# Optimization experiments

Hardware: AMD Instinct MI355X
Metric: run time of the kernel (lower is better)

The kernel has to match this reference:

```python
import jax, jax.numpy as jnp
import numpy as np

EMBED_DIM = 528
NUM_HEADS = 8
HEAD_DIM = EMBED_DIM // NUM_HEADS  # 66


def setup_inputs() -> dict:
    key = jax.random.key(0)
    k1, k2, k3, k4, k5 = jax.random.split(key, 5)
    B, D, H, W, C = 1, 16, 16, 16, EMBED_DIM
    s = 1.0 / np.sqrt(C)
    return {
        "x": jax.random.normal(k1, (B, D, H, W, C), dtype=jnp.float32),
        "w_qkv": jax.random.uniform(k2, (3 * C, C), dtype=jnp.float32, minval=-s, maxval=s),
        "b_qkv": jax.random.uniform(k3, (3 * C,), dtype=jnp.float32, minval=-s, maxval=s),
        "w_proj": jax.random.uniform(k4, (C, C), dtype=jnp.float32, minval=-s, maxval=s),
        "b_proj": jax.random.uniform(k5, (C,), dtype=jnp.float32, minval=-s, maxval=s),
    }


def reference(x, w_qkv, b_qkv, w_proj, b_proj):
    B, D, H, W, C = x.shape
    N = D * H * W
    h, hd = NUM_HEADS, HEAD_DIM
    scaling = hd ** (-0.5)

    xt = x.reshape(B, N, C)
    # qkv projection: [B, N, 3C] -> [3, B, h, N, hd]
    qkv = xt @ w_qkv.T + b_qkv
    qkv = qkv.reshape(B, N, 3, h, hd).transpose(2, 0, 3, 1, 4)
    q, k, v = qkv[0], qkv[1], qkv[2]

    # full attention over all D*H*W tokens
    attn = jnp.einsum('bhqd,bhkd->bhqk', q, k) * scaling
    attn = jax.nn.softmax(attn, axis=-1)
    out = jnp.einsum('bhqk,bhkd->bhqd', attn, v)  # [B, h, N, hd]

    out = out.transpose(0, 2, 1, 3).reshape(B, N, h * hd)
    out = out @ w_proj.T + b_proj
    return out.reshape(B, D, H, W, C)
```

## Files before the change

### kernel.cpp

```cpp
#include <hip/hip_runtime.h>

typedef __attribute__((ext_vector_type(8))) short bf16x8;
typedef __attribute__((ext_vector_type(4))) float f32x4;
typedef __attribute__((ext_vector_type(16))) float f32x16;

#define DEV __device__ __forceinline__

static constexpr int N_TOK = 4096;
static constexpr int C     = 528;
static constexpr int NH    = 8;
static constexpr int HD    = 66;
static constexpr int HDP   = 96;
static constexpr int VD96  = 96;
static constexpr int KP    = 544;
static constexpr int NQKV  = 1584;
static constexpr int NQKVP = 1632;

DEV unsigned short f2bf(float f) {
    unsigned int u = __float_as_uint(f);
    u = (u + 0x7fffu + ((u >> 16) & 1u)) >> 16;
    return (unsigned short)u;
}
DEV float bf2f(unsigned short h) { return __uint_as_float(((unsigned int)h) << 16); }
DEV unsigned cvtpk2(float a, float b) {
    unsigned r;
    asm("v_cvt_pk_bf16_f32 %0, %1, %2" : "=v"(r) : "v"(a), "v"(b));
    return r;
}
DEV void plswap(unsigned &a, unsigned &b) {
    asm volatile("v_permlane32_swap_b32 %0, %1" : "+v"(a), "+v"(b));
}

__global__ void k_prep_all(const float* __restrict__ x, const float* __restrict__ w_qkv,
                           const float* __restrict__ w_proj,
                           unsigned short* __restrict__ xb, unsigned short* __restrict__ wqkvb,
                           unsigned short* __restrict__ whi, unsigned short* __restrict__ wlo) {
    const int T0 = N_TOK * KP;
    const int T1 = T0 + NQKVP * KP;
    const int T2 = T1 + KP * KP;
    for (int idx = blockIdx.x * 256 + threadIdx.x; idx < T2; idx += gridDim.x * 256) {
        if (idx < T0) {
            int n = idx / KP, k = idx - n * KP;
            xb[idx] = (k < C) ? f2bf(x[n * C + k]) : (unsigned short)0;
        } else if (idx < T1) {
            int j = idx - T0;
            int n = j / KP, k = j - n * KP;
            wqkvb[j] = (n < NQKV && k < C) ? f2bf(w_qkv[n * C + k]) : (unsigned short)0;
        } else {
            int j = idx - T1;
            int n = j / KP, k = j - n * KP;
            unsigned short hi = 0, lo = 0;
            if (n < C && k < C) {
                float v = w_proj[n * C + k];
                hi = f2bf(v);
                lo = f2bf(v - bf2f(hi));
            }
            whi[j] = hi; wlo[j] = lo;
        }
    }
}

__launch_bounds__(256)
__global__ void k_gemm_qkv(const unsigned short* __restrict__ A,
                           const unsigned short* __restrict__ B,
                           const float* __restrict__ bias,
                           unsigned short* __restrict__ Cout) {
    constexpr int LDA = 40;
    __shared__ unsigned short Al[2][128 * LDA];
    __shared__ unsigned short Bl[2][96 * LDA];
    int tid = threadIdx.x, lane = tid & 63, wid = tid >> 6;
    int m0 = blockIdx.x * 128, n0 = blockIdx.y * 96;
    int wm = (wid >> 1) * 64, wn = (wid & 1) * 48;
    int arow0 = tid >> 2, arow1 = (256 + tid) >> 2, akc = (tid & 3) * 8;
    bool bhave = tid < 128;
    int brow1 = (256 + tid) >> 2;
    f32x4 acc[4][3] = {};
    bf16x8 ra0, ra1, rb0, rb1;

    ra0 = *(const bf16x8*)&A[(size_t)(m0 + arow0) * KP + akc];
    ra1 = *(const bf16x8*)&A[(size_t)(m0 + arow1) * KP + akc];
    rb0 = *(const bf16x8*)&B[(size_t)(n0 + arow0) * KP + akc];
    if (bhave) rb1 = *(const bf16x8*)&B[(size_t)(n0 + brow1) * KP + akc];
    *(bf16x8*)&Al[0][arow0 * LDA + akc] = ra0;
    *(bf16x8*)&Al[0][arow1 * LDA + akc] = ra1;
    *(bf16x8*)&Bl[0][arow0 * LDA + akc] = rb0;
    if (bhave) *(bf16x8*)&Bl[0][brow1 * LDA + akc] = rb1;
    __syncthreads();

    int kk = (lane >> 4) * 8, cc = lane & 15;
    for (int kt = 0; kt < 17; kt++) {
        int cur = kt & 1;
        if (kt < 16) {
            int k0 = (kt + 1) * 32;
            ra0 = *(const bf16x8*)&A[(size_t)(m0 + arow0) * KP + k0 + akc];
            ra1 = *(const bf16x8*)&A[(size_t)(m0 + arow1) * KP + k0 + akc];
            rb0 = *(const bf16x8*)&B[(size_t)(n0 + arow0) * KP + k0 + akc];
            if (bhave) rb1 = *(const bf16x8*)&B[(size_t)(n0 + brow1) * KP + k0 + akc];
        }
        bf16x8 af[4], bfr[3];
#pragma unroll
        for (int mi = 0; mi < 4; mi++) af[mi] = *(const bf16x8*)&Al[cur][(wm + mi * 16 + cc) * LDA + kk];
#pragma unroll
        for (int ni = 0; ni < 3; ni++) bfr[ni] = *(const bf16x8*)&Bl[cur][(wn + ni * 16 + cc) * LDA + kk];
#pragma unroll
        for (int mi = 0; mi < 4; mi++)
#pragma unroll
            for (int ni = 0; ni < 3; ni++)
                acc[mi][ni] = __builtin_amdgcn_mfma_f32_16x16x32_bf16(af[mi], bfr[ni], acc[mi][ni], 0, 0, 0);
        if (kt < 16) {
            int nxt = cur ^ 1;
            *(bf16x8*)&Al[nxt][arow0 * LDA + akc] = ra0;
            *(bf16x8*)&Al[nxt][arow1 * LDA + akc] = ra1;
            *(bf16x8*)&Bl[nxt][arow0 * LDA + akc] = rb0;
            if (bhave) *(bf16x8*)&Bl[nxt][brow1 * LDA + akc] = rb1;
        }
        __syncthreads();
    }
#pragma unroll
    for (int mi = 0; mi < 4; mi++)
#pragma unroll
        for (int ni = 0; ni < 3; ni++)
#pragma unroll
            for (int r = 0; r < 4; r++) {
                int row = m0 + wm + mi * 16 + (lane >> 4) * 4 + r;
                int col = n0 + wn + ni * 16 + cc;
                float v = acc[mi][ni][r] + (col < NQKV ? bias[col] : 0.f);
                Cout[(size_t)row * NQKVP + col] = f2bf(v);
            }
}

__global__ void k_reshape(const unsigned short* __restrict__ T,
                          unsigned short* __restrict__ qb, unsigned short* __restrict__ kbuf,
                          unsigned short* __restrict__ vt) {
    int h = blockIdx.y, n0 = blockIdx.x * 64, tid = threadIdx.x;
    if (blockIdx.z == 0) {
#pragma unroll
        for (int i = 0; i < 24; i++) {
            int idx = i * 256 + tid;
            int ni = idx / 96, d = idx - ni * 96;
            unsigned short zq = 0, zk = 0;
            if (d < HD) {
                zq = T[(size_t)(n0 + ni) * NQKVP + h * HD + d];
                zk = T[(size_t)(n0 + ni) * NQKVP + C + h * HD + d];
            }
            size_t a = ((size_t)h * N_TOK + n0 + ni) * HDP + d;
            qb[a] = zq; kbuf[a] = zk;
        }
    } else {
        __shared__ unsigned short lt[64 * 104];
#pragma unroll
        for (int i = 0; i < 24; i++) {
            int idx = i * 256 + tid;
            int ni = idx / 96, d = idx - ni * 96;
            unsigned short v = 0;
            if (d < HD) v = T[(size_t)(n0 + ni) * NQKVP + 2 * C + h * HD + d];
            lt[ni * 104 + d] = v;
        }
        __syncthreads();
#pragma unroll
        for (int i = 0; i < 24; i++) {
            int idx = i * 256 + tid;
            int d = idx >> 6, ni = idx & 63;
            vt[((size_t)h * VD96 + d) * N_TOK + n0 + ni] = lt[ni * 104 + d];
        }
    }
}

__launch_bounds__(512, 2)
__global__ void k_attn(const unsigned short* __restrict__ qb,
                       const unsigned short* __restrict__ kb,
                       const unsigned short* __restrict__ vt,
                       unsigned short* __restrict__ ahi,
                       unsigned short* __restrict__ alo) {
    __shared__ __align__(16) unsigned short Kl[2][128 * 128];
    __shared__ __align__(16) unsigned short Vl[2][96 * 128];
    int tid = threadIdx.x, lane = tid & 63, wid = tid >> 6;
    int wq = wid & 3, kh = wid >> 2;
    int hi = lane >> 5, lq = lane & 31;
    int bid = blockIdx.x;
    int head = bid & 7;
    int q0 = (bid >> 3) * 128;
    const float SC2 = 0.12309149097933274f * 1.4426950408889634f;

    bf16x8 aq[6];
    {
        const unsigned short* qrow = qb + ((size_t)head * N_TOK + q0 + wq * 32 + lq) * HDP + hi * 8;
#pragma unroll
        for (int t = 0; t < 6; t++) aq[t] = *(const bf16x8*)&qrow[t * 16];
    }
    f32x16 o0 = {}, o1 = {}, o2 = {};
    float m_r = -3e38f, l_r = 0.f;

    const unsigned short* kg = kb + (size_t)head * N_TOK * HDP;
    const unsigned short* vg = vt + (size_t)head * VD96 * N_TOK;

#pragma unroll
    for (int i = 0; i < 3; i++) {
        int c = i * 512 + tid;
        int row = c / 12, ch = c - row * 12;
        *(bf16x8*)&Kl[0][row * 128 + ((ch ^ (row & 15)) << 3)] =
            *(const bf16x8*)&kg[(size_t)row * HDP + ch * 8];
    }
#pragma unroll
    for (int i = 0; i < 3; i++) {
        int c = i * 512 + tid;
        int row = c >> 4, ch = c & 15;
        *(bf16x8*)&Vl[0][row * 128 + ((ch ^ (row & 15)) << 3)] =
            *(const bf16x8*)&vg[(size_t)row * N_TOK + ch * 8];
    }
    __syncthreads();

    for (int kt = 0; kt < 32; kt++) {
        int cur = kt & 1;
        bf16x8 gk[3], gv[3];
        if (kt < 31) {
            int n1 = (kt + 1) * 128;
#pragma unroll
            for (int i = 0; i < 3; i++) {
                int c = i * 512 + tid;
                int row = c / 12, ch = c - row * 12;
                gk[i] = *(const bf16x8*)&kg[(size_t)(n1 + row) * HDP + ch * 8];
            }
#pragma unroll
            for (int i = 0; i < 3; i++) {
                int c = i * 512 + tid;
                int row = c >> 4, ch = c & 15;
                gv[i] = *(const bf16x8*)&vg[(size_t)row * N_TOK + n1 + ch * 8];
            }
        }

        f32x16 s0 = {}, s1 = {};
        {
            int r0 = kh * 64 + lq, r1 = r0 + 32;
#pragma unroll
            for (int t = 0; t < 6; t++) {
                bf16x8 ka0 = *(const bf16x8*)&Kl[cur][r0 * 128 + (((2 * t + hi) ^ (r0 & 15)) << 3)];
                bf16x8 ka1 = *(const bf16x8*)&Kl[cur][r1 * 128 + (((2 * t + hi) ^ (r1 & 15)) << 3)];
                s0 = __builtin_amdgcn_mfma_f32_32x32x16_bf16(ka0, aq[t], s0, 0, 0, 0);
                s1 = __builtin_amdgcn_mfma_f32_32x32x16_bf16(ka1, aq[t], s1, 0, 0, 0);
            }
        }

        float mx = s0[0];
#pragma unroll
        for (int r = 1; r < 16; r++) mx = fmaxf(mx, s0[r]);
#pragma unroll
        for (int r = 0; r < 16; r++) mx = fmaxf(mx, s1[r]);
        mx = fmaxf(mx, __shfl_xor(mx, 32, 64));
        if (!__all((mx - m_r) * SC2 <= 8.f)) {
            float mnew = fmaxf(m_r, mx);
            float fct = __builtin_amdgcn_exp2f((m_r - mnew) * SC2);
            m_r = mnew;
            l_r *= fct;
#pragma unroll
            for (int r = 0; r < 16; r++) { o0[r] *= fct; o1[r] *= fct; o2[r] *= fct; }
        }
        float nb = m_r * SC2;
        float lsum = 0.f;
#pragma unroll
        for (int r = 0; r < 16; r++) { s0[r] = __builtin_amdgcn_exp2f(__builtin_fmaf(s0[r], SC2, -nb)); lsum += s0[r]; }
#pragma unroll
        for (int r = 0; r < 16; r++) { s1[r] = __builtin_amdgcn_exp2f(__builtin_fmaf(s1[r], SC2, -nb)); lsum += s1[r]; }
        lsum += __shfl_xor(lsum, 32, 64);
        l_r += lsum;

        unsigned u0[2][4], u1[2][4];
#pragma unroll
        for (int a = 0; a < 4; a++) {
            u0[0][a] = cvtpk2(s0[4 * a + 0], s0[4 * a + 1]);
            u1[0][a] = cvtpk2(s0[4 * a + 2], s0[4 * a + 3]);
            u0[1][a] = cvtpk2(s1[4 * a + 0], s1[4 * a + 1]);
            u1[1][a] = cvtpk2(s1[4 * a + 2], s1[4 * a + 3]);
        }
#pragma unroll
        for (int kb2 = 0; kb2 < 2; kb2++)
#pragma unroll
            for (int a0 = 0; a0 < 4; a0 += 2) {
                plswap(u0[kb2][a0], u0[kb2][a0 + 1]);
                plswap(u1[kb2][a0], u1[kb2][a0 + 1]);
            }

#pragma unroll
        for (int t2 = 0; t2 < 4; t2++) {
            int kb2 = t2 >> 1, a0 = (t2 & 1) * 2;
            union { unsigned u[4]; bf16x8 v; } pf;
            pf.u[0] = u0[kb2][a0];     pf.u[1] = u1[kb2][a0];
            pf.u[2] = u0[kb2][a0 + 1]; pf.u[3] = u1[kb2][a0 + 1];
            int ch = kh * 8 + 2 * t2 + hi;
            int rv0 = lq, rv1 = 32 + lq, rv2 = 64 + lq;
            bf16x8 va0 = *(const bf16x8*)&Vl[cur][rv0 * 128 + ((ch ^ (rv0 & 15)) << 3)];
            bf16x8 va1 = *(const bf16x8*)&Vl[cur][rv1 * 128 + ((ch ^ (rv1 & 15)) << 3)];
            bf16x8 va2 = *(const bf16x8*)&Vl[cur][rv2 * 128 + ((ch ^ (rv2 & 15)) << 3)];
            o0 = __builtin_amdgcn_mfma_f32_32x32x16_bf16(va0, pf.v, o0, 0, 0, 0);
            o1 = __builtin_amdgcn_mfma_f32_32x32x16_bf16(va1, pf.v, o1, 0, 0, 0);
            o2 = __builtin_amdgcn_mfma_f32_32x32x16_bf16(va2, pf.v, o2, 0, 0, 0);
        }

        if (kt < 31) {
            int nxt = cur ^ 1;
#pragma unroll
            for (int i = 0; i < 3; i++) {
                int c = i * 512 + tid;
                int row = c / 12, ch = c - row * 12;
                *(bf16x8*)&Kl[nxt][row * 128 + ((ch ^ (row & 15)) << 3)] = gk[i];
            }
#pragma unroll
            for (int i = 0; i < 3; i++) {
                int c = i * 512 + tid;
                int row = c >> 4, ch = c & 15;
                *(bf16x8*)&Vl[nxt][row * 128 + ((ch ^ (row & 15)) << 3)] = gv[i];
            }
        }
        __syncthreads();
    }

    float* xc = (float*)&Kl[0][0];
    float* rg = xc + (size_t)(wq * 64 + lane) * 52;
    if (kh == 1) {
#pragma unroll
        for (int r = 0; r < 16; r++) rg[r] = o0[r];
#pragma unroll
        for (int r = 0; r < 16; r++) rg[16 + r] = o1[r];
#pragma unroll
        for (int r = 0; r < 16; r++) rg[32 + r] = o2[r];
        rg[48] = m_r; rg[49] = l_r;
    }
    __syncthreads();
    if (kh == 0) {
        float m1 = rg[48], l1 = rg[49];
        float m12 = fmaxf(m_r, m1);
        float f0 = __builtin_amdgcn_exp2f((m_r - m12) * SC2);
        float f1 = __builtin_amdgcn_exp2f((m1 - m12) * SC2);
        float inv = 1.f / (l_r * f0 + l1 * f1);
        int token = q0 + wq * 32 + lq;
#pragma unroll
        for (int db = 0; db < 3; db++) {
#pragma unroll
            for (int r = 0; r < 16; r++) {
                int d = db * 32 + (r & 3) + 8 * (r >> 2) + 4 * hi;
                if (d < HD) {
                    float own = (db == 0) ? o0[r] : (db == 1) ? o1[r] : o2[r];
                    float val = (own * f0 + rg[db * 16 + r] * f1) * inv;
                    unsigned short hb = f2bf(val);
                    float lo = val - bf2f(hb);
                    size_t a = (size_t)token * KP + head * HD + d;
                    ahi[a] = hb; alo[a] = f2bf(lo);
                }
            }
        }
    }
}

__launch_bounds__(256)
__global__ void k_gemm_proj(const unsigned short* __restrict__ Ahi_, const unsigned short* __restrict__ Alo_,
                            const unsigned short* __restrict__ Whi_, const unsigned short* __restrict__ Wlo_,
                            const float* __restrict__ bias, float* __restrict__ out) {
    constexpr int LDA = 40;
    __shared__ unsigned short Ah[2][128 * LDA], Aw[2][128 * LDA];
    __shared__ unsigned short Bh[2][64 * LDA],  Bw[2][64 * LDA];
    int tid = threadIdx.x, lane = tid & 63, wid = tid >> 6;
    int m0 = blockIdx.x * 128, n0 = blockIdx.y * 64;
    int wm = wid * 32;
    int arow0 = tid >> 2, arow1 = (256 + tid) >> 2, akc = (tid & 3) * 8;
    bool bok = (n0 + arow0) < KP;
    f32x4 acc[2][4] = {};
    bf16x8 rah0, rah1, ral0, ral1, rbh, rbl;
    const bf16x8 zero8 = {};

    rah0 = *(const bf16x8*)&Ahi_[(size_t)(m0 + arow0) * KP + akc];
    rah1 = *(const bf16x8*)&Ahi_[(size_t)(m0 + arow1) * KP + akc];
    ral0 = *(const bf16x8*)&Alo_[(size_t)(m0 + arow0) * KP + akc];
    ral1 = *(const bf16x8*)&Alo_[(size_t)(m0 + arow1) * KP + akc];
    rbh = bok ? *(const bf16x8*)&Whi_[(size_t)(n0 + arow0) * KP + akc] : zero8;
    rbl = bok ? *(const bf16x8*)&Wlo_[(size_t)(n0 + arow0) * KP + akc] : zero8;
    *(bf16x8*)&Ah[0][arow0 * LDA + akc] = rah0;
    *(bf16x8*)&Ah[0][arow1 * LDA + akc] = rah1;
    *(bf16x8*)&Aw[0][arow0 * LDA + akc] = ral0;
    *(bf16x8*)&Aw[0][arow1 * LDA + akc] = ral1;
    *(bf16x8*)&Bh[0][arow0 * LDA + akc] = rbh;
    *(bf16x8*)&Bw[0][arow0 * LDA + akc] = rbl;
    __syncthreads();

    int kk = (lane >> 4) * 8, cc = lane & 15;
    for (int kt = 0; kt < 17; kt++) {
        int cur = kt & 1;
        if (kt < 16) {
            int k0 = (kt + 1) * 32;
            rah0 = *(const bf16x8*)&Ahi_[(size_t)(m0 + arow0) * KP + k0 + akc];
            rah1 = *(const bf16x8*)&Ahi_[(size_t)(m0 + arow1) * KP + k0 + akc];
            ral0 = *(const bf16x8*)&Alo_[(size_t)(m0 + arow0) * KP + k0 + akc];
            ral1 = *(const bf16x8*)&Alo_[(size_t)(m0 + arow1) * KP + k0 + akc];
            rbh = bok ? *(const bf16x8*)&Whi_[(size_t)(n0 + arow0) * KP + k0 + akc] : zero8;
            rbl = bok ? *(const bf16x8*)&Wlo_[(size_t)(n0 + arow0) * KP + k0 + akc] : zero8;
        }
        bf16x8 ah[2], al[2], bh[4], bl[4];
#pragma unroll
        for (int mi = 0; mi < 2; mi++) {
            ah[mi] = *(const bf16x8*)&Ah[cur][(wm + mi * 16 + cc) * LDA + kk];
            al[mi] = *(const bf16x8*)&Aw[cur][(wm + mi * 16 + cc) * LDA + kk];
        }
#pragma unroll
        for (int ni = 0; ni < 4; ni++) {
            bh[ni] = *(const bf16x8*)&Bh[cur][(ni * 16 + cc) * LDA + kk];
            bl[ni] = *(const bf16x8*)&Bw[cur][(ni * 16 + cc) * LDA + kk];
        }
#pragma unroll
        for (int mi = 0; mi < 2; mi++)
#pragma unroll
            for (int ni = 0; ni < 4; ni++) {
                acc[mi][ni] = __builtin_amdgcn_mfma_f32_16x16x32_bf16(ah[mi], bh[ni], acc[mi][ni], 0, 0, 0);
                acc[mi][ni] = __builtin_amdgcn_mfma_f32_16x16x32_bf16(ah[mi], bl[ni], acc[mi][ni], 0, 0, 0);
                acc[mi][ni] = __builtin_amdgcn_mfma_f32_16x16x32_bf16(al[mi], bh[ni], acc[mi][ni], 0, 0, 0);
            }
        if (kt < 16) {
            int nxt = cur ^ 1;
            *(bf16x8*)&Ah[nxt][arow0 * LDA + akc] = rah0;
            *(bf16x8*)&Ah[nxt][arow1 * LDA + akc] = rah1;
            *(bf16x8*)&Aw[nxt][arow0 * LDA + akc] = ral0;
            *(bf16x8*)&Aw[nxt][arow1 * LDA + akc] = ral1;
            *(bf16x8*)&Bh[nxt][arow0 * LDA + akc] = rbh;
            *(bf16x8*)&Bw[nxt][arow0 * LDA + akc] = rbl;
        }
        __syncthreads();
    }
#pragma unroll
    for (int mi = 0; mi < 2; mi++)
#pragma unroll
        for (int ni = 0; ni < 4; ni++)
#pragma unroll
            for (int r = 0; r < 4; r++) {
                int row = m0 + wm + mi * 16 + (lane >> 4) * 4 + r;
                int col = n0 + ni * 16 + cc;
                if (col < C) out[(size_t)row * C + col] = acc[mi][ni][r] + bias[col];
            }
}

extern "C" void kernel_launch(void* const* d_in, const int* in_sizes, int n_in,
                              void* d_out, int out_size, void* d_ws, size_t ws_size,
                              hipStream_t stream) {
    const float* x      = (const float*)d_in[0];
    const float* w_qkv  = (const float*)d_in[1];
    const float* b_qkv  = (const float*)d_in[2];
    const float* w_proj = (const float*)d_in[3];
    const float* b_proj = (const float*)d_in[4];
    float* out = (float*)d_out;
    char* ws = (char*)d_ws;

    const size_t o_xb     = 0;
    const size_t o_wqkvb  = o_xb     + 4456448;
    const size_t o_whi    = o_wqkvb  + 1775616;
    const size_t o_wlo    = o_whi    + 591872;
    const size_t o_qkvtmp = o_wlo    + 591872;
    const size_t o_qbf    = o_qkvtmp + 13369344;
    const size_t o_kbf    = o_qbf    + 6291456;
    const size_t o_vt     = o_kbf    + 6291456;
    const size_t need     = o_vt + 6291456;
    if (ws_size < need) return;

    unsigned short* xb     = (unsigned short*)(ws + o_xb);
    unsigned short* wqkvb  = (unsigned short*)(ws + o_wqkvb);
    unsigned short* whi    = (unsigned short*)(ws + o_whi);
    unsigned short* wlo    = (unsigned short*)(ws + o_wlo);
    unsigned short* qkvtmp = (unsigned short*)(ws + o_qkvtmp);
    unsigned short* qbf    = (unsigned short*)(ws + o_qbf);
    unsigned short* kbf    = (unsigned short*)(ws + o_kbf);
    unsigned short* vt     = (unsigned short*)(ws + o_vt);
    unsigned short* ahi    = xb;
    unsigned short* alo    = qkvtmp;

    k_prep_all  <<<2048, 256, 0, stream>>>(x, w_qkv, w_proj, xb, wqkvb, whi, wlo);
    k_gemm_qkv  <<<dim3(N_TOK / 128, NQKVP / 96), 256, 0, stream>>>(xb, wqkvb, b_qkv, qkvtmp);
    k_reshape   <<<dim3(N_TOK / 64, NH, 2), 256, 0, stream>>>(qkvtmp, qbf, kbf, vt);
    k_attn      <<<dim3(256), 512, 0, stream>>>(qbf, kbf, vt, ahi, alo);
    k_gemm_proj <<<dim3(N_TOK / 128, 9), 256, 0, stream>>>(ahi, alo, whi, wlo, b_proj, out);
}
```

Baseline: 124.1 us.

## Scatter Q/K directly from QKV GEMM and split attention keys across 16 waves

After: 152.0 us. 22.5% more time.

```diff
diff --git a/kernel.cpp b/kernel.cpp
--- a/kernel.cpp
+++ b/kernel.cpp
@@ -34,11 +34,13 @@
 __global__ void k_prep_all(const float* __restrict__ x, const float* __restrict__ w_qkv,
                            const float* __restrict__ w_proj,
                            unsigned short* __restrict__ xb, unsigned short* __restrict__ wqkvb,
-                           unsigned short* __restrict__ whi, unsigned short* __restrict__ wlo) {
+                           unsigned short* __restrict__ whi, unsigned short* __restrict__ wlo,
+                           unsigned short* __restrict__ qb, unsigned short* __restrict__ kbuf) {
     const int T0 = N_TOK * KP;
     const int T1 = T0 + NQKVP * KP;
     const int T2 = T1 + KP * KP;
-    for (int idx = blockIdx.x * 256 + threadIdx.x; idx < T2; idx += gridDim.x * 256) {
+    const int T3 = T2 + NH * N_TOK * (HDP - HD);
+    for (int idx = blockIdx.x * 256 + threadIdx.x; idx < T3; idx += gridDim.x * 256) {
         if (idx < T0) {
             int n = idx / KP, k = idx - n * KP;
             xb[idx] = (k < C) ? f2bf(x[n * C + k]) : (unsigned short)0;
@@ -46,7 +48,7 @@
             int j = idx - T0;
             int n = j / KP, k = j - n * KP;
             wqkvb[j] = (n < NQKV && k < C) ? f2bf(w_qkv[n * C + k]) : (unsigned short)0;
-        } else {
+        } else if (idx < T2) {
             int j = idx - T1;
             int n = j / KP, k = j - n * KP;
             unsigned short hi = 0, lo = 0;
@@ -56,6 +58,11 @@
                 lo = f2bf(v - bf2f(hi));
             }
             whi[j] = hi; wlo[j] = lo;
+        } else {
+            int j = idx - T2;
+            int n = j / 30, p = j - 30 * n;
+            size_t a = (size_t)n * HDP + HD + p;
+            qb[a] = 0; kbuf[a] = 0;
         }
     }
 }
@@ -64,7 +71,8 @@
 __global__ void k_gemm_qkv(const unsigned short* __restrict__ A,
                            const unsigned short* __restrict__ B,
                            const float* __restrict__ bias,
-                           unsigned short* __restrict__ Cout) {
+                           unsigned short* __restrict__ qb, unsigned short* __restrict__ kbuf,
+                           unsigned short* __restrict__ vtmp) {
     constexpr int LDA = 40;
     __shared__ unsigned short Al[2][128 * LDA];
     __shared__ unsigned short Bl[2][96 * LDA];
@@ -125,55 +133,46 @@
                 int row = m0 + wm + mi * 16 + (lane >> 4) * 4 + r;
                 int col = n0 + wn + ni * 16 + cc;
                 float v = acc[mi][ni][r] + (col < NQKV ? bias[col] : 0.f);
-                Cout[(size_t)row * NQKVP + col] = f2bf(v);
-            }
-}
-
-__global__ void k_reshape(const unsigned short* __restrict__ T,
-                          unsigned short* __restrict__ qb, unsigned short* __restrict__ kbuf,
-                          unsigned short* __restrict__ vt) {
+                unsigned short b = f2bf(v);
+                if (col < 2 * C) {
+                    int d5 = (col >= C) ? col - C : col;
+                    unsigned h = (unsigned)d5 / 66u;
+                    int dd = d5 - 66 * (int)h;
+                    size_t a = ((size_t)h * N_TOK + row) * HDP + dd;
+                    if (col >= C) kbuf[a] = b; else qb[a] = b;
+                } else if (col < NQKV) {
+                    vtmp[(size_t)row * C + (col - 2 * C)] = b;
+                }
+            }
+}
+
+__global__ void k_reshape_v(const unsigned short* __restrict__ vtmp, unsigned short* __restrict__ vt) {
+    __shared__ unsigned short lt[64 * 104];
     int h = blockIdx.y, n0 = blockIdx.x * 64, tid = threadIdx.x;
-    if (blockIdx.z == 0) {
-#pragma unroll
-        for (int i = 0; i < 24; i++) {
-            int idx = i * 256 + tid;
-            int ni = idx / 96, d = idx - ni * 96;
-            unsigned short zq = 0, zk = 0;
-            if (d < HD) {
-                zq = T[(size_t)(n0 + ni) * NQKVP + h * HD + d];
-                zk = T[(size_t)(n0 + ni) * NQKVP + C + h * HD + d];
-            }
-            size_t a = ((size_t)h * N_TOK + n0 + ni) * HDP + d;
-            qb[a] = zq; kbuf[a] = zk;
-        }
-    } else {
-        __shared__ unsigned short lt[64 * 104];
-#pragma unroll
-        for (int i = 0; i < 24; i++) {
-            int idx = i * 256 + tid;
-            int ni = idx / 96, d = idx - ni * 96;
-            unsigned short v = 0;
-            if (d < HD) v = T[(size_t)(n0 + ni) * NQKVP + 2 * C + h * HD + d];
-            lt[ni * 104 + d] = v;
-        }
-        __syncthreads();
-#pragma unroll
-        for (int i = 0; i < 24; i++) {
-            int idx = i * 256 + tid;
-            int d = idx >> 6, ni = idx & 63;
-            vt[((size_t)h * VD96 + d) * N_TOK + n0 + ni] = lt[ni * 104 + d];
-        }
-    }
-}
-
-__launch_bounds__(512, 2)
+#pragma unroll
+    for (int i = 0; i < 24; i++) {
+        int idx = i * 256 + tid;
+        int ni = idx / 96, d = idx - ni * 96;
+        unsigned short v = 0;
+        if (d < HD) v = vtmp[(size_t)(n0 + ni) * C + h * HD + d];
+        lt[ni * 104 + d] = v;
+    }
+    __syncthreads();
+#pragma unroll
+    for (int i = 0; i < 24; i++) {
+        int idx = i * 256 + tid;
+        int d = idx >> 6, ni = idx & 63;
+        vt[((size_t)h * VD96 + d) * N_TOK + n0 + ni] = lt[ni * 104 + d];
+    }
+}
+
+__launch_bounds__(1024, 4)
 __global__ void k_attn(const unsigned short* __restrict__ qb,
                        const unsigned short* __restrict__ kb,
                        const unsigned short* __restrict__ vt,
                        unsigned short* __restrict__ ahi,
                        unsigned short* __restrict__ alo) {
-    __shared__ __align__(16) unsigned short Kl[2][128 * 128];
-    __shared__ __align__(16) unsigned short Vl[2][96 * 128];
+    __shared__ __align__(16) unsigned short S[2][128 * 128 + 96 * 128];
     int tid = threadIdx.x, lane = tid & 63, wid = tid >> 6;
     int wq = wid & 3, kh = wid >> 2;
     int hi = lane >> 5, lq = lane & 31;
@@ -194,58 +193,53 @@
     const unsigned short* kg = kb + (size_t)head * N_TOK * HDP;
     const unsigned short* vg = vt + (size_t)head * VD96 * N_TOK;
 
-#pragma unroll
-    for (int i = 0; i < 3; i++) {
-        int c = i * 512 + tid;
-        int row = c / 12, ch = c - row * 12;
-        *(bf16x8*)&Kl[0][row * 128 + ((ch ^ (row & 15)) << 3)] =
-            *(const bf16x8*)&kg[(size_t)row * HDP + ch * 8];
-    }
-#pragma unroll
-    for (int i = 0; i < 3; i++) {
-        int c = i * 512 + tid;
-        int row = c >> 4, ch = c & 15;
-        *(bf16x8*)&Vl[0][row * 128 + ((ch ^ (row & 15)) << 3)] =
-            *(const bf16x8*)&vg[(size_t)row * N_TOK + ch * 8];
+    const unsigned short* gptr[3];
+    int gstep[3], laddr[3];
+#pragma unroll
+    for (int j = 0; j < 3; j++) {
+        int c = j * 1024 + tid;
+        if (c < 1536) {
+            int row = c / 12, ch = c - row * 12;
+            gptr[j] = kg + (size_t)row * HDP + ch * 8;
+            gstep[j] = 128 * HDP;
+            laddr[j] = row * 128 + ((ch ^ (row & 15)) << 3);
+        } else {
+            int c2 = c - 1536;
+            int row = c2 >> 4, ch = c2 & 15;
+            gptr[j] = vg + (size_t)row * N_TOK + ch * 8;
+            gstep[j] = 128;
+            laddr[j] = 128 * 128 + row * 128 + ((ch ^ (row & 15)) << 3);
+        }
+    }
+#pragma unroll
+    for (int j = 0; j < 3; j++) {
+        *(bf16x8*)&S[0][laddr[j]] = *(const bf16x8*)gptr[j];
+        gptr[j] += gstep[j];
     }
     __syncthreads();
 
     for (int kt = 0; kt < 32; kt++) {
         int cur = kt & 1;
-        bf16x8 gk[3], gv[3];
+        bf16x8 g[3];
         if (kt < 31) {
-            int n1 = (kt + 1) * 128;
-#pragma unroll
-            for (int i = 0; i < 3; i++) {
-                int c = i * 512 + tid;
-                int row = c / 12, ch = c - row * 12;
-                gk[i] = *(const bf16x8*)&kg[(size_t)(n1 + row) * HDP + ch * 8];
-            }
-#pragma unroll
-            for (int i = 0; i < 3; i++) {
-                int c = i * 512 + tid;
-                int row = c >> 4, ch = c & 15;
-                gv[i] = *(const bf16x8*)&vg[(size_t)row * N_TOK + n1 + ch * 8];
-            }
-        }
-
-        f32x16 s0 = {}, s1 = {};
+#pragma unroll
+            for (int j = 0; j < 3; j++) { g[j] = *(const bf16x8*)gptr[j]; gptr[j] += gstep[j]; }
+        }
+
+        f32x16 s0 = {};
         {
-            int r0 = kh * 64 + lq, r1 = r0 + 32;
+            int r0 = kh * 32 + lq;
+            const unsigned short* Kc = &S[cur][0];
 #pragma unroll
             for (int t = 0; t < 6; t++) {
-                bf16x8 ka0 = *(const bf16x8*)&Kl[cur][r0 * 128 + (((2 * t + hi) ^ (r0 & 15)) << 3)];
-                bf16x8 ka1 = *(const bf16x8*)&Kl[cur][r1 * 128 + (((2 * t + hi) ^ (r1 & 15)) << 3)];
-                s0 = __builtin_amdgcn_mfma_f32_32x32x16_bf16(ka0, aq[t], s0, 0, 0, 0);
-                s1 = __builtin_amdgcn_mfma_f32_32x32x16_bf16(ka1, aq[t], s1, 0, 0, 0);
+                bf16x8 ka = *(const bf16x8*)&Kc[r0 * 128 + (((2 * t + hi) ^ (r0 & 15)) << 3)];
+                s0 = __builtin_amdgcn_mfma_f32_32x32x16_bf16(ka, aq[t], s0, 0, 0, 0);
             }
         }
 
         float mx = s0[0];
 #pragma unroll
         for (int r = 1; r < 16; r++) mx = fmaxf(mx, s0[r]);
-#pragma unroll
-        for (int r = 0; r < 16; r++) mx = fmaxf(mx, s1[r]);
         mx = fmaxf(mx, __shfl_xor(mx, 32, 64));
         if (!__all((mx - m_r) * SC2 <= 8.f)) {
             float mnew = fmaxf(m_r, mx);
@@ -259,92 +253,98 @@
         float lsum = 0.f;
 #pragma unroll
         for (int r = 0; r < 16; r++) { s0[r] = __builtin_amdgcn_exp2f(__builtin_fmaf(s0[r], SC2, -nb)); lsum += s0[r]; }
-#pragma unroll
-        for (int r = 0; r < 16; r++) { s1[r] = __builtin_amdgcn_exp2f(__builtin_fmaf(s1[r], SC2, -nb)); lsum += s1[r]; }
         lsum += __shfl_xor(lsum, 32, 64);
         l_r += lsum;
 
-        unsigned u0[2][4], u1[2][4];
+        unsigned u0[4], u1[4];
 #pragma unroll
         for (int a = 0; a < 4; a++) {
-            u0[0][a] = cvtpk2(s0[4 * a + 0], s0[4 * a + 1]);
-            u1[0][a] = cvtpk2(s0[4 * a + 2], s0[4 * a + 3]);
-            u0[1][a] = cvtpk2(s1[4 * a + 0], s1[4 * a + 1]);
-            u1[1][a] = cvtpk2(s1[4 * a + 2], s1[4 * a + 3]);
-        }
-#pragma unroll
-        for (int kb2 = 0; kb2 < 2; kb2++)
-#pragma unroll
-            for (int a0 = 0; a0 < 4; a0 += 2) {
-                plswap(u0[kb2][a0], u0[kb2][a0 + 1]);
-                plswap(u1[kb2][a0], u1[kb2][a0 + 1]);
-            }
-
-#pragma unroll
-        for (int t2 = 0; t2 < 4; t2++) {
-            int kb2 = t2 >> 1, a0 = (t2 & 1) * 2;
-            union { unsigned u[4]; bf16x8 v; } pf;
-            pf.u[0] = u0[kb2][a0];     pf.u[1] = u1[kb2][a0];
-            pf.u[2] = u0[kb2][a0 + 1]; pf.u[3] = u1[kb2][a0 + 1];
-            int ch = kh * 8 + 2 * t2 + hi;
-            int rv0 = lq, rv1 = 32 + lq, rv2 = 64 + lq;
-            bf16x8 va0 = *(const bf16x8*)&Vl[cur][rv0 * 128 + ((ch ^ (rv0 & 15)) << 3)];
-            bf16x8 va1 = *(const bf16x8*)&Vl[cur][rv1 * 128 + ((ch ^ (rv1 & 15)) << 3)];
-            bf16x8 va2 = *(const bf16x8*)&Vl[cur][rv2 * 128 + ((ch ^ (rv2 & 15)) << 3)];
-            o0 = __builtin_amdgcn_mfma_f32_32x32x16_bf16(va0, pf.v, o0, 0, 0, 0);
-            o1 = __builtin_amdgcn_mfma_f32_32x32x16_bf16(va1, pf.v, o1, 0, 0, 0);
-            o2 = __builtin_amdgcn_mfma_f32_32x32x16_bf16(va2, pf.v, o2, 0, 0, 0);
+            u0[a] = cvtpk2(s0[4 * a + 0], s0[4 * a + 1]);
+            u1[a] = cvtpk2(s0[4 * a + 2], s0[4 * a + 3]);
+        }
+        plswap(u0[0], u0[1]); plswap(u0[2], u0[3]);
+        plswap(u1[0], u1[1]); plswap(u1[2], u1[3]);
+
+        {
+            const unsigned short* Vc = &S[cur][128 * 128];
+#pragma unroll
+            for (int t2 = 0; t2 < 2; t2++) {
+                int a0 = t2 * 2;
+                union { unsigned u[4]; bf16x8 v; } pf;
+                pf.u[0] = u0[a0];     pf.u[1] = u1[a0];
+                pf.u[2] = u0[a0 + 1]; pf.u[3] = u1[a0 + 1];
+                int ch = kh * 4 + 2 * t2 + hi;
+                int rv0 = lq, rv1 = 32 + lq, rv2 = 64 + lq;
+                bf16x8 va0 = *(const bf16x8*)&Vc[rv0 * 128 + ((ch ^ (rv0 & 15)) << 3)];
+                bf16x8 va1 = *(const bf16x8*)&Vc[rv1 * 128 + ((ch ^ (rv1 & 15)) << 3)];
+                bf16x8 va2 = *(const bf16x8*)&Vc[rv2 * 128 + ((ch ^ (rv2 & 15)) << 3)];
+                o0 = __builtin_amdgcn_mfma_f32_32x32x16_bf16(va0, pf.v, o0, 0, 0, 0);
+                o1 = __builtin_amdgcn_mfma_f32_32x32x16_bf16(va1, pf.v, o1, 0, 0, 0);
+                o2 = __builtin_amdgcn_mfma_f32_32x32x16_bf16(va2, pf.v, o2, 0, 0, 0);
+            }
         }
 
         if (kt < 31) {
             int nxt = cur ^ 1;
 #pragma unroll
-            for (int i = 0; i < 3; i++) {
-                int c = i * 512 + tid;
-                int row = c / 12, ch = c - row * 12;
-                *(bf16x8*)&Kl[nxt][row * 128 + ((ch ^ (row & 15)) << 3)] = gk[i];
-            }
-#pragma unroll
-            for (int i = 0; i < 3; i++) {
-                int c = i * 512 + tid;
-                int row = c >> 4, ch = c & 15;
-                *(bf16x8*)&Vl[nxt][row * 128 + ((ch ^ (row & 15)) << 3)] = gv[i];
-            }
-        }
-        __syncthreads();
-    }
-
-    float* xc = (float*)&Kl[0][0];
-    float* rg = xc + (size_t)(wq * 64 + lane) * 52;
-    if (kh == 1) {
-#pragma unroll
-        for (int r = 0; r < 16; r++) rg[r] = o0[r];
-#pragma unroll
-        for (int r = 0; r < 16; r++) rg[16 + r] = o1[r];
-#pragma unroll
-        for (int r = 0; r < 16; r++) rg[32 + r] = o2[r];
-        rg[48] = m_r; rg[49] = l_r;
-    }
-    __syncthreads();
-    if (kh == 0) {
-        float m1 = rg[48], l1 = rg[49];
-        float m12 = fmaxf(m_r, m1);
-        float f0 = __builtin_amdgcn_exp2f((m_r - m12) * SC2);
-        float f1 = __builtin_amdgcn_exp2f((m1 - m12) * SC2);
-        float inv = 1.f / (l_r * f0 + l1 * f1);
-        int token = q0 + wq * 32 + lq;
-#pragma unroll
-        for (int db = 0; db < 3; db++) {
+            for (int j = 0; j < 3; j++) *(bf16x8*)&S[nxt][laddr[j]] = g[j];
+        }
+        __syncthreads();
+    }
+
+    float* xc = (float*)&S[0][0];
+    {
+        float* rg = xc + (size_t)((wq * 2 + (kh & 1)) * 64 + lane) * 53;
+        if (kh >= 2) {
+#pragma unroll
+            for (int r = 0; r < 16; r++) { rg[r] = o0[r]; rg[16 + r] = o1[r]; rg[32 + r] = o2[r]; }
+            rg[48] = m_r; rg[49] = l_r;
+        }
+        __syncthreads();
+        if (kh < 2) {
+            float m1 = rg[48], l1 = rg[49];
+            float m12 = fmaxf(m_r, m1);
+            float f0 = __builtin_amdgcn_exp2f((m_r - m12) * SC2);
+            float f1 = __builtin_amdgcn_exp2f((m1 - m12) * SC2);
+            l_r = l_r * f0 + l1 * f1;
+            m_r = m12;
 #pragma unroll
             for (int r = 0; r < 16; r++) {
-                int d = db * 32 + (r & 3) + 8 * (r >> 2) + 4 * hi;
-                if (d < HD) {
-                    float own = (db == 0) ? o0[r] : (db == 1) ? o1[r] : o2[r];
-                    float val = (own * f0 + rg[db * 16 + r] * f1) * inv;
-                    unsigned short hb = f2bf(val);
-                    float lo = val - bf2f(hb);
-                    size_t a = (size_t)token * KP + head * HD + d;
-                    ahi[a] = hb; alo[a] = f2bf(lo);
+                o0[r] = o0[r] * f0 + rg[r] * f1;
+                o1[r] = o1[r] * f0 + rg[16 + r] * f1;
+                o2[r] = o2[r] * f0 + rg[32 + r] * f1;
+            }
+        }
+        __syncthreads();
+    }
+    {
+        float* rg = xc + (size_t)(wq * 64 + lane) * 53;
+        if (kh == 1) {
+#pragma unroll
+            for (int r = 0; r < 16; r++) { rg[r] = o0[r]; rg[16 + r] = o1[r]; rg[32 + r] = o2[r]; }
+            rg[48] = m_r; rg[49] = l_r;
+        }
+        __syncthreads();
+        if (kh == 0) {
+            float m1 = rg[48], l1 = rg[49];
+            float m12 = fmaxf(m_r, m1);
+            float f0 = __builtin_amdgcn_exp2f((m_r - m12) * SC2);
+            float f1 = __builtin_amdgcn_exp2f((m1 - m12) * SC2);
+            float inv = 1.f / (l_r * f0 + l1 * f1);
+            int token = q0 + wq * 32 + lq;
+#pragma unroll
+            for (int db = 0; db < 3; db++) {
+#pragma unroll
+                for (int r = 0; r < 16; r++) {
+                    int d = db * 32 + (r & 3) + 8 * (r >> 2) + 4 * hi;
+                    if (d < HD) {
+                        float own = (db == 0) ? o0[r] : (db == 1) ? o1[r] : o2[r];
+                        float val = (own * f0 + rg[db * 16 + r] * f1) * inv;
+                        unsigned short hb = f2bf(val);
+                        float lo = val - bf2f(hb);
+                        size_t a = (size_t)token * KP + head * HD + d;
+                        ahi[a] = hb; alo[a] = f2bf(lo);
+                    }
                 }
             }
         }
@@ -446,31 +446,31 @@
     float* out = (float*)d_out;
     char* ws = (char*)d_ws;
 
-    const size_t o_xb     = 0;
-    const size_t o_wqkvb  = o_xb     + 4456448;
-    const size_t o_whi    = o_wqkvb  + 1775616;
-    const size_t o_wlo    = o_whi    + 591872;
-    const size_t o_qkvtmp = o_wlo    + 591872;
-    const size_t o_qbf    = o_qkvtmp + 13369344;
-    const size_t o_kbf    = o_qbf    + 6291456;
-    const size_t o_vt     = o_kbf    + 6291456;
-    const size_t need     = o_vt + 6291456;
+    const size_t o_xb    = 0;
+    const size_t o_wqkvb = o_xb    + 4456448;
+    const size_t o_whi   = o_wqkvb + 1775616;
+    const size_t o_wlo   = o_whi   + 591872;
+    const size_t o_vtmp  = o_wlo   + 591872;
+    const size_t o_qbf   = o_vtmp  + 4456448;
+    const size_t o_kbf   = o_qbf   + 6291456;
+    const size_t o_vt    = o_kbf   + 6291456;
+    const size_t need    = o_vt + 6291456;
     if (ws_size < need) return;
 
-    unsigned short* xb     = (unsigned short*)(ws + o_xb);
-    unsigned short* wqkvb  = (unsigned short*)(ws + o_wqkvb);
-    unsigned short* whi    = (unsigned short*)(ws + o_whi);
-    unsigned short* wlo    = (unsigned short*)(ws + o_wlo);
-    unsigned short* qkvtmp = (unsigned short*)(ws + o_qkvtmp);
-    unsigned short* qbf    = (unsigned short*)(ws + o_qbf);
-    unsigned short* kbf    = (unsigned short*)(ws + o_kbf);
-    unsigned short* vt     = (unsigned short*)(ws + o_vt);
-    unsigned short* ahi    = xb;
-    unsigned short* alo    = qkvtmp;
-
-    k_prep_all  <<<2048, 256, 0, stream>>>(x, w_qkv, w_proj, xb, wqkvb, whi, wlo);
-    k_gemm_qkv  <<<dim3(N_TOK / 128, NQKVP / 96), 256, 0, stream>>>(xb, wqkvb, b_qkv, qkvtmp);
-    k_reshape   <<<dim3(N_TOK / 64, NH, 2), 256, 0, stream>>>(qkvtmp, qbf, kbf, vt);
-    k_attn      <<<dim3(256), 512, 0, stream>>>(qbf, kbf, vt, ahi, alo);
+    unsigned short* xb    = (unsigned short*)(ws + o_xb);
+    unsigned short* wqkvb = (unsigned short*)(ws + o_wqkvb);
+    unsigned short* whi   = (unsigned short*)(ws + o_whi);
+    unsigned short* wlo   = (unsigned short*)(ws + o_wlo);
+    unsigned short* vtmp  = (unsigned short*)(ws + o_vtmp);
+    unsigned short* qbf   = (unsigned short*)(ws + o_qbf);
+    unsigned short* kbf   = (unsigned short*)(ws + o_kbf);
+    unsigned short* vt    = (unsigned short*)(ws + o_vt);
+    unsigned short* ahi   = xb;
+    unsigned short* alo   = vtmp;
+
+    k_prep_all  <<<2048, 256, 0, stream>>>(x, w_qkv, w_proj, xb, wqkvb, whi, wlo, qbf, kbf);
+    k_gemm_qkv  <<<dim3(N_TOK / 128, NQKVP / 96), 256, 0, stream>>>(xb, wqkvb, b_qkv, qbf, kbf, vtmp);
+    k_reshape_v <<<dim3(N_TOK / 64, NH), 256, 0, stream>>>(vtmp, vt);
+    k_attn      <<<dim3(256), 1024, 0, stream>>>(qbf, kbf, vt, ahi, alo);
     k_gemm_proj <<<dim3(N_TOK / 128, 9), 256, 0, stream>>>(ahi, alo, whi, wlo, b_proj, out);
 }
```
